# Kernel optimization log

Measured on AMD Instinct MI355X. Metric: run time of the kernel, lower is better.

The kernel has to match this reference:

```python
import jax, jax.numpy as jnp
import numpy as np

D_MODEL = 1024
N_HEADS = 16
HEAD_DIM = D_MODEL // N_HEADS
B, L, E = 2, 2048, 256


def _linear_params(key, d_out, d_in):
    kw, kb = jax.random.split(key)
    lim = 1.0 / np.sqrt(d_in)
    W = jax.random.uniform(kw, (d_out, d_in), jnp.float32, -lim, lim)
    b = jax.random.uniform(kb, (d_out,), jnp.float32, -lim, lim)
    return W, b


def setup_inputs() -> dict:
    key = jax.random.key(0)
    ks = jax.random.split(key, 10)
    x = jax.random.normal(ks[0], (B, L, D_MODEL), jnp.float32)
    kg_embeds = jax.random.normal(ks[1], (B, E, D_MODEL), jnp.float32)
    Wq, bq = _linear_params(ks[2], D_MODEL, D_MODEL)
    Wk, bk = _linear_params(ks[3], D_MODEL, D_MODEL)
    Wv, bv = _linear_params(ks[4], D_MODEL, D_MODEL)
    Wo, bo = _linear_params(ks[5], D_MODEL, D_MODEL)
    Wkk, bkk = _linear_params(ks[6], D_MODEL, D_MODEL)
    Wkv, bkv = _linear_params(ks[7], D_MODEL, D_MODEL)
    Wg, bg = _linear_params(ks[8], D_MODEL, 2 * D_MODEL)
    return {"x": x, "kg_embeds": kg_embeds,
            "Wq": Wq, "bq": bq, "Wk": Wk, "bk": bk, "Wv": Wv, "bv": bv,
            "Wkk": Wkk, "bkk": bkk, "Wkv": Wkv, "bkv": bkv,
            "Wo": Wo, "bo": bo, "Wg": Wg, "bg": bg}


def _heads(t):
    # [B, S, D] -> [B, H, S, hd]
    Bb, S, _ = t.shape
    return t.reshape(Bb, S, N_HEADS, HEAD_DIM).transpose(0, 2, 1, 3)


def reference(x, kg_embeds, Wq, bq, Wk, bk, Wv, bv, Wkk, bkk, Wkv, bkv, Wo, bo, Wg, bg):
    scale = HEAD_DIM ** -0.5
    q = _heads(x @ Wq.T + bq)                      # [B,H,L,hd]
    k = _heads(x @ Wk.T + bk)
    v = _heads(x @ Wv.T + bv)
    k_kg = _heads(kg_embeds @ Wkk.T + bkk)         # [B,H,E,hd]
    v_kg = _heads(kg_embeds @ Wkv.T + bkv)
    k_aug = jnp.concatenate([k, k_kg], axis=2)     # [B,H,L+E,hd]
    v_aug = jnp.concatenate([v, v_kg], axis=2)
    scores = jnp.einsum('bhld,bhmd->bhlm', q, k_aug) * scale  # [B,H,L,L+E]
    attn = jax.nn.softmax(scores, axis=-1)
    out = jnp.einsum('bhlm,bhmd->bhld', attn, v_aug)           # [B,H,L,hd]
    out = out.transpose(0, 2, 1, 3).reshape(x.shape)            # [B,L,D]
    kg_global = jnp.broadcast_to(kg_embeds.mean(axis=1, keepdims=True), x.shape)
    gate = jax.nn.sigmoid(jnp.concatenate([out, kg_global], axis=-1) @ Wg.T + bg)
    return gate * (out @ Wo.T + bo) + (1.0 - gate) * x
```

## Files before the change

### kernel.cpp

```cpp
#include <hip/hip_runtime.h>
#include <stdint.h>

typedef unsigned short ushort_t;
typedef __attribute__((ext_vector_type(8))) short short8;
typedef __attribute__((ext_vector_type(4))) short short4v;
typedef __attribute__((ext_vector_type(4))) float f32x4;
typedef __attribute__((ext_vector_type(4))) unsigned uintx4;

#define DEV static __device__ __forceinline__

DEV unsigned short f2bf(float f) {
  unsigned u = __builtin_bit_cast(unsigned, f);
  u += 0x7fffu + ((u >> 16) & 1u);
  return (unsigned short)(u >> 16);
}
DEV float bf2f(unsigned short b) {
  return __builtin_bit_cast(float, (unsigned)b << 16);
}

DEV void gl16(const void* g, void* l) {
  __builtin_amdgcn_global_load_lds(
      (__attribute__((address_space(1))) char*)(unsigned long long)g,
      (__attribute__((address_space(3))) char*)(unsigned)(unsigned long long)l,
      16, 0, 0);
}

DEV f32x4 mfma_bf16(short8 a, short8 b, f32x4 c) {
  return __builtin_amdgcn_mfma_f32_16x16x32_bf16(a, b, c, 0, 0, 0);
}

DEV unsigned cvtpk(float lo, float hi) {
  unsigned r;
  asm("v_cvt_pk_bf16_f32 %0, %1, %2" : "=v"(r) : "v"(lo), "v"(hi));
  return r;
}
DEV void swap_net(unsigned& a, unsigned& b) {
  asm("v_permlane32_swap_b32 %0, %1" : "+v"(a), "+v"(b));
  asm("v_permlane16_swap_b32 %0, %1" : "+v"(a), "+v"(b));
}
DEV float redmax4(float x) {
  unsigned a = __builtin_bit_cast(unsigned, x), b = a;
  asm("v_permlane16_swap_b32 %0, %1" : "+v"(a), "+v"(b));
  float y = fmaxf(__builtin_bit_cast(float, a), __builtin_bit_cast(float, b));
  unsigned c = __builtin_bit_cast(unsigned, y), d = c;
  asm("v_permlane32_swap_b32 %0, %1" : "+v"(c), "+v"(d));
  return fmaxf(__builtin_bit_cast(float, c), __builtin_bit_cast(float, d));
}
DEV float lanebcast(float v, int srclane) {
  return __builtin_bit_cast(float,
      __builtin_amdgcn_ds_bpermute(srclane * 4, __builtin_bit_cast(int, v)));
}

__global__ __launch_bounds__(256) void k_cvt_all(
    const float* __restrict__ x, const float* __restrict__ kg,
    const float* __restrict__ Wq, const float* __restrict__ Wk, const float* __restrict__ Wv,
    const float* __restrict__ Wkk, const float* __restrict__ Wkv,
    const float* __restrict__ Wo, const float* __restrict__ Wg,
    ushort_t* __restrict__ xh, ushort_t* __restrict__ kgh,
    ushort_t* __restrict__ WB1, ushort_t* __restrict__ WB2, ushort_t* __restrict__ WB3) {
  const int b = blockIdx.x;
  if (b >= 10752) {
    const int i = (b - 10752) * 256 + threadIdx.x;
    const int r = i >> 8, c = (i & 255) * 4;
    const float4 v = *(const float4*)(Wg + (size_t)r * 2048 + c);
    short4v o;
    o.x = (short)f2bf(v.x); o.y = (short)f2bf(v.y); o.z = (short)f2bf(v.z); o.w = (short)f2bf(v.w);
    *(short4v*)(WB3 + 1048576 + (size_t)r * 1024 + c) = o;
    return;
  }
  const float* src;
  ushort_t* dst;
  int off;
  if (b < 4096)       { src = x;   dst = xh;            off = b; }
  else if (b < 4608)  { src = kg;  dst = kgh;           off = b - 4096; }
  else if (b < 5632)  { src = Wq;  dst = WB1;           off = b - 4608; }
  else if (b < 6656)  { src = Wk;  dst = WB1 + 1048576; off = b - 5632; }
  else if (b < 7680)  { src = Wv;  dst = WB1 + 2097152; off = b - 6656; }
  else if (b < 8704)  { src = Wkk; dst = WB2;           off = b - 7680; }
  else if (b < 9728)  { src = Wkv; dst = WB2 + 1048576; off = b - 8704; }
  else                { src = Wo;  dst = WB3;           off = b - 9728; }
  const int i = off * 1024 + threadIdx.x * 4;
  const float4 v = *(const float4*)(src + i);
  short4v o;
  o.x = (short)f2bf(v.x); o.y = (short)f2bf(v.y); o.z = (short)f2bf(v.z); o.w = (short)f2bf(v.w);
  *(short4v*)(dst + i) = o;
}

__global__ __launch_bounds__(256) void k_kgmean(const float* __restrict__ kg, float* __restrict__ out) {
  const int i = blockIdx.x * 256 + threadIdx.x;
  const int b = i >> 10, d = i & 1023;
  float s = 0.f;
  #pragma unroll 4
  for (int e = 0; e < 256; e++) s += kg[((size_t)b * 256 + e) * 1024 + d];
  out[i] = s * (1.0f / 256.0f);
}

__global__ __launch_bounds__(256) void k_g2(const float* __restrict__ kgm, const float* __restrict__ Wg,
                                            const float* __restrict__ bg, float* __restrict__ g2) {
  const int w = threadIdx.x >> 6, l = threadIdx.x & 63;
  const int idx = blockIdx.x * 4 + w;
  const int b = idx >> 10, n = idx & 1023;
  const float* wr = Wg + (size_t)n * 2048 + 1024;
  const float* mb = kgm + b * 1024;
  float s = 0.f;
  #pragma unroll
  for (int j = 0; j < 16; j++) s += mb[j * 64 + l] * wr[j * 64 + l];
  #pragma unroll
  for (int m = 32; m >= 1; m >>= 1) s += __shfl_xor(s, m);
  if (l == 0) g2[idx] = s + bg[n];
}

__global__ __launch_bounds__(256, 3) void k_mm128(
    const ushort_t* __restrict__ A0, const ushort_t* __restrict__ B0,
    const ushort_t* __restrict__ A1, const ushort_t* __restrict__ B1,
    const float* __restrict__ f0, const float* __restrict__ f1, const float* __restrict__ f2,
    const float* __restrict__ f3, const float* __restrict__ f4,
    ushort_t* __restrict__ o0, ushort_t* __restrict__ o1, ushort_t* __restrict__ o2) {
  __shared__ __align__(16) char SHb[49152];
  const int tid = threadIdx.x;
  const int w = tid >> 6, l = tid & 63;
  const int wr = w >> 1, wc = w & 1;
  const int fr = l & 15, fg = l >> 4;

  int m0, n0, iskg = 0;
  {
    const int wg = ((int)blockIdx.x & 7) * 104 + ((int)blockIdx.x >> 3);
    if (wg < 768) { m0 = (wg / 24) * 128; n0 = (wg % 24) * 128; }
    else          { const int k = wg - 768; iskg = 1; m0 = (k >> 4) * 128; n0 = (k & 15) * 128; }
  }
  const ushort_t* A = iskg ? A1 : A0;
  const ushort_t* B = iskg ? B1 : B0;

  int grow[2], gcb[2];
  #pragma unroll
  for (int j = 0; j < 2; j++) {
    const int beta = j * 256 + tid;
    const int rp = beta >> 3;
    const int u = (beta & 7) ^ (rp & 7);
    grow[j] = 2 * rp + (u >> 2);
    gcb[j] = u & 3;
  }
  const char* gA[2];
  const char* gB[2];
  #pragma unroll
  for (int j = 0; j < 2; j++) {
    gA[j] = (const char*)A + (size_t)(m0 + grow[j]) * 2048 + gcb[j] * 16;
    gB[j] = (const char*)B + (size_t)(n0 + grow[j]) * 2048 + gcb[j] * 16;
  }

  auto stage = [&](int s, int kt) {
    char* As = SHb + s * 16384;
    char* Bs = As + 8192;
    const int ko = kt * 64;
    #pragma unroll
    for (int j = 0; j < 2; j++) {
      gl16(gA[j] + ko, As + j * 4096 + tid * 16);
      gl16(gB[j] + ko, Bs + j * 4096 + tid * 16);
    }
  };

  int aoff[4], boff[4];
  #pragma unroll
  for (int i = 0; i < 4; i++) {
    const int rowa = wr * 64 + i * 16 + fr;
    aoff[i] = (rowa >> 1) * 128 + ((((rowa & 1) << 6) | (fg << 4)) ^ (((rowa >> 1) & 7) << 4));
    const int rowb = wc * 64 + i * 16 + fr;
    boff[i] = (rowb >> 1) * 128 + ((((rowb & 1) << 6) | (fg << 4)) ^ (((rowb >> 1) & 7) << 4));
  }

  f32x4 acc[4][4] = {};

  stage(0, 0);
  stage(1, 1);
  int sc = 0, sn2 = 2;
  for (int kt = 0; kt < 32; kt++) {
    if (kt < 31) asm volatile("s_waitcnt vmcnt(4)" ::: "memory");
    else         asm volatile("s_waitcnt vmcnt(0)" ::: "memory");
    __builtin_amdgcn_s_barrier();
    asm volatile("" ::: "memory");
    if (kt < 30) stage(sn2, kt + 2);
    const char* Ab = SHb + sc * 16384;
    const char* Bb = Ab + 8192;
    short8 af[4], bf[4];
    #pragma unroll
    for (int j = 0; j < 4; j++) bf[j] = *(const short8*)(Bb + boff[j]);
    #pragma unroll
    for (int i = 0; i < 4; i++) af[i] = *(const short8*)(Ab + aoff[i]);
    __builtin_amdgcn_s_setprio(1);
    #pragma unroll
    for (int i = 0; i < 4; i++)
      #pragma unroll
      for (int j = 0; j < 4; j++)
        acc[i][j] = mfma_bf16(af[i], bf[j], acc[i][j]);
    __builtin_amdgcn_s_setprio(0);
    sc++; if (sc == 3) sc = 0;
    sn2++; if (sn2 == 3) sn2 = 0;
  }
  __syncthreads();

  const int sec = n0 >> 10;
  const bool isV = (!iskg && sec == 2) || (iskg && sec == 1);

  if (isV) {
    ushort_t* SHs = (ushort_t*)SHb;
    const float* bV = iskg ? f4 : f2;
    const int bidx = iskg ? (m0 >> 8) : (m0 >> 11);
    const int colbase = iskg ? (2048 + (m0 & 255)) : (m0 & 2047);
    #pragma unroll
    for (int i = 0; i < 4; i++) {
      #pragma unroll
      for (int j = 0; j < 4; j++) {
        const int nl = wc * 64 + j * 16 + fr;
        const int ml0 = wr * 64 + i * 16 + fg * 4;
        const float bb = bV[(n0 & 1023) + nl];
        short4v pk;
        #pragma unroll
        for (int r = 0; r < 4; r++) pk[r] = (short)f2bf(acc[i][j][r] + bb);
        *(short4v*)(SHs + nl * 128 + (ml0 ^ ((nl & 7) << 3))) = pk;
      }
    }
    __syncthreads();
    const int row = tid >> 1, half = tid & 1;
    const int h = ((n0 & 1023) >> 6) + (row >> 6);
    const int d = row & 63;
    ushort_t* dst = o2 + ((size_t)(bidx * 16 + h) * 64 + d) * 2304 + colbase + half * 64;
    const ushort_t* srow2 = SHs + row * 128;
    #pragma unroll
    for (int k2 = 0; k2 < 8; k2++) {
      const int me = (half * 64 + k2 * 8) ^ ((row & 7) << 3);
      *(short8*)(dst + k2 * 8) = *(const short8*)(srow2 + me);
    }
    return;
  }

  #pragma unroll
  for (int i = 0; i < 4; i++) {
    #pragma unroll
    for (int j = 0; j < 4; j++) {
      const int nn = (n0 & 1023) + wc * 64 + j * 16 + fr;
      const int h = nn >> 6, d = nn & 63;
      #pragma unroll
      for (int r = 0; r < 4; r++) {
        const int m = m0 + wr * 64 + i * 16 + fg * 4 + r;
        const float v = acc[i][j][r];
        if (iskg) {
          const int b = m >> 8, e = m & 255;
          o1[((size_t)(b * 16 + h) * 2304 + 2048 + e) * 64 + d] = f2bf(v + f3[nn]);
        } else if (sec == 0) {
          const int b = m >> 11, lq = m & 2047;
          o0[((size_t)(b * 16 + h) * 2048 + lq) * 64 + d] = f2bf((v + f0[nn]) * 0.18033688f);
        } else {
          const int b = m >> 11, lq = m & 2047;
          o1[((size_t)(b * 16 + h) * 2304 + lq) * 64 + d] = f2bf(v + f1[nn]);
        }
      }
    }
  }
}

__global__ __launch_bounds__(256, 2) void k_mmout(
    const ushort_t* __restrict__ Og, const ushort_t* __restrict__ WB3,
    const float* __restrict__ bo, const float* __restrict__ g2v,
    const float* __restrict__ x, float* __restrict__ y) {
  __shared__ __align__(16) char SHb[61440];
  const int tid = threadIdx.x;
  const int w = tid >> 6, l = tid & 63;
  const int wr = w >> 1, wc = w & 1;
  const int fr = l & 15, fg = l >> 4;

  const int wg = ((int)blockIdx.x & 7) * 64 + ((int)blockIdx.x >> 3);
  const int m0 = (wg >> 3) * 64, n0 = (wg & 7) * 128;

  const int rpA = tid >> 3, uA = (tid & 7) ^ (rpA & 7);
  const char* gAp = (const char*)Og + (size_t)(m0 + 2 * rpA + (uA >> 2)) * 2048 + (uA & 3) * 16;
  int grow[2], gcb[2];
  #pragma unroll
  for (int j = 0; j < 2; j++) {
    const int beta = j * 256 + tid;
    const int rp = beta >> 3;
    const int u = (beta & 7) ^ (rp & 7);
    grow[j] = 2 * rp + (u >> 2);
    gcb[j] = u & 3;
  }
  const char* gBo[2];
  const char* gBg[2];
  #pragma unroll
  for (int j = 0; j < 2; j++) {
    gBo[j] = (const char*)WB3 + (size_t)(n0 + grow[j]) * 2048 + gcb[j] * 16;
    gBg[j] = (const char*)(WB3 + 1048576) + (size_t)(n0 + grow[j]) * 2048 + gcb[j] * 16;
  }

  auto stage = [&](int s, int kt) {
    char* As = SHb + s * 20480;
    const int ko = kt * 64;
    gl16(gAp + ko, As + tid * 16);
    #pragma unroll
    for (int j = 0; j < 2; j++) {
      gl16(gBo[j] + ko, As + 4096 + j * 4096 + tid * 16);
      gl16(gBg[j] + ko, As + 12288 + j * 4096 + tid * 16);
    }
  };

  int aoff[2], boff[4];
  #pragma unroll
  for (int i = 0; i < 2; i++) {
    const int rowa = wr * 32 + i * 16 + fr;
    aoff[i] = (rowa >> 1) * 128 + ((((rowa & 1) << 6) | (fg << 4)) ^ (((rowa >> 1) & 7) << 4));
  }
  #pragma unroll
  for (int j = 0; j < 4; j++) {
    const int rowb = wc * 64 + j * 16 + fr;
    boff[j] = (rowb >> 1) * 128 + ((((rowb & 1) << 6) | (fg << 4)) ^ (((rowb >> 1) & 7) << 4));
  }

  f32x4 ao[2][4] = {};
  f32x4 ag[2][4] = {};

  stage(0, 0);
  stage(1, 1);
  int sc = 0, sn2 = 2;
  for (int kt = 0; kt < 32; kt++) {
    if (kt < 31) asm volatile("s_waitcnt vmcnt(5)" ::: "memory");
    else         asm volatile("s_waitcnt vmcnt(0)" ::: "memory");
    __builtin_amdgcn_s_barrier();
    asm volatile("" ::: "memory");
    if (kt < 30) stage(sn2, kt + 2);
    const char* Ab = SHb + sc * 20480;
    short8 af[2], bof[4], bgf[4];
    #pragma unroll
    for (int i = 0; i < 2; i++) af[i] = *(const short8*)(Ab + aoff[i]);
    #pragma unroll
    for (int j = 0; j < 4; j++) {
      bof[j] = *(const short8*)(Ab + 4096 + boff[j]);
      bgf[j] = *(const short8*)(Ab + 12288 + boff[j]);
    }
    __builtin_amdgcn_s_setprio(1);
    #pragma unroll
    for (int i = 0; i < 2; i++)
      #pragma unroll
      for (int j = 0; j < 4; j++) {
        ao[i][j] = mfma_bf16(af[i], bof[j], ao[i][j]);
        ag[i][j] = mfma_bf16(af[i], bgf[j], ag[i][j]);
      }
    __builtin_amdgcn_s_setprio(0);
    sc++; if (sc == 3) sc = 0;
    sn2++; if (sn2 == 3) sn2 = 0;
  }

  const int bidx = m0 >> 11;
  #pragma unroll
  for (int i = 0; i < 2; i++) {
    #pragma unroll
    for (int j = 0; j < 4; j++) {
      const int nn = n0 + wc * 64 + j * 16 + fr;
      const float bb = bo[nn];
      const float gg = g2v[bidx * 1024 + nn];
      #pragma unroll
      for (int r = 0; r < 4; r++) {
        const int m = m0 + wr * 32 + i * 16 + fg * 4 + r;
        const float co = ao[i][j][r] + bb;
        const float cg = ag[i][j][r] + gg;
        const float gate = 1.0f / (1.0f + __builtin_amdgcn_exp2f(cg * -1.4426950408889634f));
        const float xv = x[(size_t)m * 1024 + nn];
        y[(size_t)m * 1024 + nn] = xv + gate * (co - xv);
      }
    }
  }
}

__global__ __launch_bounds__(256, 4) void k_attn(
    const ushort_t* __restrict__ Qg, const ushort_t* __restrict__ Kg,
    const ushort_t* __restrict__ Vtg, ushort_t* __restrict__ Og) {
  __shared__ __align__(16) ushort_t Ks[2][64 * 64];
  __shared__ __align__(16) ushort_t Vs[2][64 * 64];
  const int tid = threadIdx.x;
  const int w = tid >> 6, l = tid & 63;
  const int fr = l & 15, fg = l >> 4;

  const int id = blockIdx.y * gridDim.x + blockIdx.x;
  const int bh = (id & 7) * 4 + ((id >> 3) >> 5);
  const int q0 = ((id >> 3) & 31) * 64 + w * 16;

  short8 qf[2];
  {
    const short* qrow = (const short*)(Qg + ((size_t)bh * 2048 + q0 + fr) * 64);
    qf[0] = *(const short8*)(qrow + fg * 8);
    qf[1] = *(const short8*)(qrow + 32 + fg * 8);
  }

  constexpr short ONE = 0x3F80;
  const short8 ones = {ONE, ONE, ONE, ONE, ONE, ONE, ONE, ONE};

  f32x4 o[4] = {};
  f32x4 lacc = {};
  float mrun = -1.0e30f;

  const int rsub = tid >> 3;
  const int cS = ((tid & 7) * 16) ^ ((rsub & 7) << 4);
  const char* kbase = (const char*)(Kg + (size_t)bh * 2304 * 64);
  const char* vbase = (const char*)(Vtg + (size_t)bh * 64 * 2304);

  auto stage = [&](int nb, int tile) {
    #pragma unroll
    for (int j = 0; j < 2; j++) {
      const int row = j * 32 + rsub;
      gl16(kbase + (size_t)(tile * 64 + row) * 128 + cS,
           (char*)&Ks[nb][0] + j * 4096 + tid * 16);
      gl16(vbase + (size_t)row * 4608 + tile * 128 + cS,
           (char*)&Vs[nb][0] + j * 4096 + tid * 16);
    }
  };

  stage(0, 0);

  const int rswz = (fr & 7) << 4;

  for (int mt = 0; mt < 36; mt++) {
    __syncthreads();
    if (mt < 35) stage((mt + 1) & 1, mt + 1);

    const char* Kb = (const char*)&Ks[mt & 1][0];
    const char* Vb = (const char*)&Vs[mt & 1][0];

    f32x4 s[4];
    #pragma unroll
    for (int t = 0; t < 4; t++) {
      const int rb = (t * 16 + fr) * 128 + fg * 16;
      const short8 k0 = *(const short8*)(Kb + (rb ^ rswz));
      const short8 k1 = *(const short8*)(Kb + ((rb + 64) ^ rswz));
      f32x4 z = {};
      z = mfma_bf16(k0, qf[0], z);
      z = mfma_bf16(k1, qf[1], z);
      s[t] = z;
    }

    float m = fmaxf(s[0][0], s[0][1]);
    m = fmaxf(fmaxf(m, s[0][2]), s[0][3]);
    m = fmaxf(fmaxf(m, s[1][0]), s[1][1]);
    m = fmaxf(fmaxf(m, s[1][2]), s[1][3]);
    m = fmaxf(fmaxf(m, s[2][0]), s[2][1]);
    m = fmaxf(fmaxf(m, s[2][2]), s[2][3]);
    m = fmaxf(fmaxf(m, s[3][0]), s[3][1]);
    m = fmaxf(fmaxf(m, s[3][2]), s[3][3]);
    const float mx = redmax4(m);
    if (__any(mx - mrun > 11.5416f)) {
      const float mn = fmaxf(mrun, mx);
      const float al = __builtin_amdgcn_exp2f(mrun - mn);
      mrun = mn;
      float ab[4];
      #pragma unroll
      for (int r = 0; r < 4; r++) ab[r] = lanebcast(al, fg * 4 + r);
      #pragma unroll
      for (int r = 0; r < 4; r++) {
        lacc[r] *= ab[r];
        #pragma unroll
        for (int dt = 0; dt < 4; dt++) o[dt][r] *= ab[r];
      }
    }
    #pragma unroll
    for (int t = 0; t < 4; t++)
      #pragma unroll
      for (int r = 0; r < 4; r++)
        s[t][r] = __builtin_amdgcn_exp2f(s[t][r] - mrun);

    #pragma unroll
    for (int c = 0; c < 2; c++) {
      unsigned a0 = cvtpk(s[2 * c][0], s[2 * c][1]);
      unsigned b0 = cvtpk(s[2 * c + 1][0], s[2 * c + 1][1]);
      unsigned a1 = cvtpk(s[2 * c][2], s[2 * c][3]);
      unsigned b1 = cvtpk(s[2 * c + 1][2], s[2 * c + 1][3]);
      swap_net(a0, b0);
      swap_net(a1, b1);
      uintx4 u;
      u.x = a0; u.y = a1; u.z = b0; u.w = b1;
      const short8 pf = __builtin_bit_cast(short8, u);
      lacc = mfma_bf16(pf, ones, lacc);
      #pragma unroll
      for (int dt = 0; dt < 4; dt++) {
        const int vb2 = ((dt * 16 + fr) * 128) + fg * 16 + c * 64;
        const short8 vf = *(const short8*)(Vb + (vb2 ^ rswz));
        o[dt] = mfma_bf16(pf, vf, o[dt]);
      }
    }
  }

  const int b = bh >> 4, h = bh & 15;
  #pragma unroll
  for (int r = 0; r < 4; r++) {
    const float inv = 1.0f / lacc[r];
    const int q = q0 + fg * 4 + r;
    ushort_t* orow = Og + ((size_t)b * 2048 + q) * 1024 + h * 64;
    #pragma unroll
    for (int dt = 0; dt < 4; dt++) orow[dt * 16 + fr] = f2bf(o[dt][r] * inv);
  }
}

extern "C" void kernel_launch(void* const* d_in, const int* in_sizes, int n_in,
                              void* d_out, int out_size, void* d_ws, size_t ws_size,
                              hipStream_t stream) {
  (void)in_sizes; (void)n_in; (void)out_size; (void)ws_size;
  const float* x   = (const float*)d_in[0];
  const float* kg  = (const float*)d_in[1];
  const float* Wq  = (const float*)d_in[2];
  const float* bq  = (const float*)d_in[3];
  const float* Wk  = (const float*)d_in[4];
  const float* bk  = (const float*)d_in[5];
  const float* Wv  = (const float*)d_in[6];
  const float* bv  = (const float*)d_in[7];
  const float* Wkk = (const float*)d_in[8];
  const float* bkk = (const float*)d_in[9];
  const float* Wkv = (const float*)d_in[10];
  const float* bkv = (const float*)d_in[11];
  const float* Wo  = (const float*)d_in[12];
  const float* bo  = (const float*)d_in[13];
  const float* Wg  = (const float*)d_in[14];
  const float* bg  = (const float*)d_in[15];
  float* y = (float*)d_out;

  char* ws = (char*)d_ws;
  size_t off = 0;
  auto take = [&](size_t bytes) {
    char* p = ws + off;
    off += (bytes + 255) & ~(size_t)255;
    return p;
  };
  ushort_t* xh   = (ushort_t*)take((size_t)4096 * 1024 * 2);
  ushort_t* kgh  = (ushort_t*)take((size_t)512 * 1024 * 2);
  ushort_t* WB1  = (ushort_t*)take((size_t)3072 * 1024 * 2);
  ushort_t* WB2  = (ushort_t*)take((size_t)2048 * 1024 * 2);
  ushort_t* WB3  = (ushort_t*)take((size_t)2048 * 1024 * 2);
  ushort_t* Qg   = (ushort_t*)take((size_t)32 * 2048 * 64 * 2);
  ushort_t* Kaug = (ushort_t*)take((size_t)32 * 2304 * 64 * 2);
  ushort_t* Vt   = (ushort_t*)take((size_t)32 * 2304 * 64 * 2);
  ushort_t* Og   = (ushort_t*)take((size_t)4096 * 1024 * 2);
  float* kgm     = (float*)take(2048 * 4);
  float* g2      = (float*)take(2048 * 4);

  k_cvt_all<<<11776, 256, 0, stream>>>(x, kg, Wq, Wk, Wv, Wkk, Wkv, Wo, Wg,
                                       xh, kgh, WB1, WB2, WB3);
  k_kgmean<<<8, 256, 0, stream>>>(kg, kgm);
  k_g2<<<512, 256, 0, stream>>>(kgm, Wg, bg, g2);

  k_mm128<<<832, 256, 0, stream>>>(xh, WB1, kgh, WB2,
                                   bq, bk, bv, bkk, bkv, Qg, Kaug, Vt);
  k_attn<<<dim3(32, 32), 256, 0, stream>>>(Qg, Kaug, Vt, Og);
  k_mmout<<<512, 256, 0, stream>>>(Og, WB3, bo, g2, x, y);
}
```

Before: 177.1 us.

## Replace QKV projection GEMM with 256x256-tile, 8-wave, double-buffered pipelined kernel

Rewrites the fused Q/K/V/KG projection GEMM to use 256x256 output tiles with 512 threads (8 waves, each computing 128x64), a K-step of 64 with double-buffered 64KB LDS stages, and LDS reads interleaved with MFMA quads and global-to-LDS loads under fine-grained barriers. Larger tiles raise arithmetic intensity and cut global/L2 traffic, and the interleaved schedule is meant to overlap loads with compute. The cost is a grid of only 208 blocks on a 256-CU device, so some CUs sit idle. It also uses 128KB of LDS per block and many barriers per iteration, which limits occupancy.

```diff
diff --git a/kernel.cpp b/kernel.cpp
--- a/kernel.cpp
+++ b/kernel.cpp
@@ -110,148 +110,191 @@
   if (l == 0) g2[idx] = s + bg[n];
 }
 
-__global__ __launch_bounds__(256, 3) void k_mm128(
-    const ushort_t* __restrict__ A0, const ushort_t* __restrict__ B0,
-    const ushort_t* __restrict__ A1, const ushort_t* __restrict__ B1,
-    const float* __restrict__ f0, const float* __restrict__ f1, const float* __restrict__ f2,
-    const float* __restrict__ f3, const float* __restrict__ f4,
-    ushort_t* __restrict__ o0, ushort_t* __restrict__ o1, ushort_t* __restrict__ o2) {
-  __shared__ __align__(16) char SHb[49152];
+#define BARm() do { __builtin_amdgcn_s_barrier(); asm volatile("" ::: "memory"); } while (0)
+
+#define RD_A(DST, SBASE, IOFF)                                      \
+  _Pragma("unroll")                                                 \
+  for (int i = 0; i < 4; i++) {                                     \
+    DST[i][0] = *(const short8*)((SBASE) + aoff[(IOFF) + i]);       \
+    DST[i][1] = *(const short8*)((SBASE) + (aoff[(IOFF) + i] ^ 64));\
+  }
+#define RD_B(DST, SBASE, JOFF)                                      \
+  _Pragma("unroll")                                                 \
+  for (int j = 0; j < 2; j++) {                                     \
+    DST[j][0] = *(const short8*)((SBASE) + boff[(JOFF) + j]);       \
+    DST[j][1] = *(const short8*)((SBASE) + (boff[(JOFF) + j] ^ 64));\
+  }
+#define MFMA_QUAD(AF, BF, I0, J0)                                   \
+  __builtin_amdgcn_s_setprio(1);                                    \
+  _Pragma("unroll")                                                 \
+  for (int i = 0; i < 4; i++) {                                     \
+    _Pragma("unroll")                                               \
+    for (int j = 0; j < 2; j++) {                                   \
+      acc[(I0) + i][(J0) + j] = mfma_bf16(AF[i][0], BF[j][0], acc[(I0) + i][(J0) + j]); \
+      acc[(I0) + i][(J0) + j] = mfma_bf16(AF[i][1], BF[j][1], acc[(I0) + i][(J0) + j]); \
+    }                                                               \
+  }                                                                 \
+  __builtin_amdgcn_s_setprio(0);
+
+__global__ __launch_bounds__(512, 2) void k_mmqkv(
+    const ushort_t* __restrict__ xh, const ushort_t* __restrict__ WB1,
+    const ushort_t* __restrict__ kgh, const ushort_t* __restrict__ WB2,
+    const float* __restrict__ bq, const float* __restrict__ bk, const float* __restrict__ bv,
+    const float* __restrict__ bkk, const float* __restrict__ bkv,
+    ushort_t* __restrict__ Qg, ushort_t* __restrict__ Kaug, ushort_t* __restrict__ Vt) {
+  __shared__ __align__(16) char SHb[131072];
   const int tid = threadIdx.x;
   const int w = tid >> 6, l = tid & 63;
-  const int wr = w >> 1, wc = w & 1;
+  const int wr = w >> 2, wc = w & 3;
   const int fr = l & 15, fg = l >> 4;
 
-  int m0, n0, iskg = 0;
-  {
-    const int wg = ((int)blockIdx.x & 7) * 104 + ((int)blockIdx.x >> 3);
-    if (wg < 768) { m0 = (wg / 24) * 128; n0 = (wg % 24) * 128; }
-    else          { const int k = wg - 768; iskg = 1; m0 = (k >> 4) * 128; n0 = (k & 15) * 128; }
-  }
-  const ushort_t* A = iskg ? A1 : A0;
-  const ushort_t* B = iskg ? B1 : B0;
-
-  int grow[2], gcb[2];
-  #pragma unroll
-  for (int j = 0; j < 2; j++) {
-    const int beta = j * 256 + tid;
-    const int rp = beta >> 3;
-    const int u = (beta & 7) ^ (rp & 7);
-    grow[j] = 2 * rp + (u >> 2);
-    gcb[j] = u & 3;
-  }
-  const char* gA[2];
-  const char* gB[2];
-  #pragma unroll
-  for (int j = 0; j < 2; j++) {
-    gA[j] = (const char*)A + (size_t)(m0 + grow[j]) * 2048 + gcb[j] * 16;
-    gB[j] = (const char*)B + (size_t)(n0 + grow[j]) * 2048 + gcb[j] * 16;
-  }
-
-  auto stage = [&](int s, int kt) {
-    char* As = SHb + s * 16384;
-    char* Bs = As + 8192;
-    const int ko = kt * 64;
-    #pragma unroll
-    for (int j = 0; j < 2; j++) {
-      gl16(gA[j] + ko, As + j * 4096 + tid * 16);
-      gl16(gB[j] + ko, Bs + j * 4096 + tid * 16);
-    }
+  int m0, by, iskg = 0;
+  const int wg = ((int)blockIdx.x & 7) * 26 + ((int)blockIdx.x >> 3);
+  if (wg < 192) { m0 = (wg / 12) * 256; by = wg % 12; }
+  else          { const int k = wg - 192; iskg = 1; by = k & 7; m0 = (k >> 3) * 256; }
+  const int n0 = by * 256;
+  const ushort_t* A = iskg ? kgh : xh;
+  const ushort_t* B = iskg ? WB2 : WB1;
+
+  const int rIH = tid >> 3;
+  const int cc = (tid & 7) ^ (rIH & 7);
+  const char* gA = (const char*)A + (size_t)(m0 + rIH) * 2048 + cc * 16;
+  const char* gB = (const char*)B + (size_t)(n0 + rIH) * 2048 + cc * 16;
+
+  auto stg = [&](int slot, int ab, int h, int kt) {
+    const char* g = (ab ? gB : gA) + (size_t)h * 262144 + kt * 128;
+    char* d = SHb + (slot << 16) + ab * 32768 + h * 16384 + tid * 16;
+    gl16(g, d);
+    gl16(g + 131072, d + 8192);
   };
 
-  int aoff[4], boff[4];
-  #pragma unroll
-  for (int i = 0; i < 4; i++) {
-    const int rowa = wr * 64 + i * 16 + fr;
-    aoff[i] = (rowa >> 1) * 128 + ((((rowa & 1) << 6) | (fg << 4)) ^ (((rowa >> 1) & 7) << 4));
-    const int rowb = wc * 64 + i * 16 + fr;
-    boff[i] = (rowb >> 1) * 128 + ((((rowb & 1) << 6) | (fg << 4)) ^ (((rowb >> 1) & 7) << 4));
-  }
-
-  f32x4 acc[4][4] = {};
-
-  stage(0, 0);
-  stage(1, 1);
-  int sc = 0, sn2 = 2;
-  for (int kt = 0; kt < 32; kt++) {
-    if (kt < 31) asm volatile("s_waitcnt vmcnt(4)" ::: "memory");
-    else         asm volatile("s_waitcnt vmcnt(0)" ::: "memory");
-    __builtin_amdgcn_s_barrier();
-    asm volatile("" ::: "memory");
-    if (kt < 30) stage(sn2, kt + 2);
-    const char* Ab = SHb + sc * 16384;
-    const char* Bb = Ab + 8192;
-    short8 af[4], bf[4];
-    #pragma unroll
-    for (int j = 0; j < 4; j++) bf[j] = *(const short8*)(Bb + boff[j]);
-    #pragma unroll
-    for (int i = 0; i < 4; i++) af[i] = *(const short8*)(Ab + aoff[i]);
-    __builtin_amdgcn_s_setprio(1);
-    #pragma unroll
-    for (int i = 0; i < 4; i++)
-      #pragma unroll
-      for (int j = 0; j < 4; j++)
-        acc[i][j] = mfma_bf16(af[i], bf[j], acc[i][j]);
-    __builtin_amdgcn_s_setprio(0);
-    sc++; if (sc == 3) sc = 0;
-    sn2++; if (sn2 == 3) sn2 = 0;
+  const int swz = (fg ^ (fr & 7)) * 16;
+  int aoff[8], boff[4];
+  #pragma unroll
+  for (int i = 0; i < 8; i++)
+    aoff[i] = wr * 16384 + (i * 16 + fr) * 128 + swz;
+  #pragma unroll
+  for (int j = 0; j < 4; j++)
+    boff[j] = 32768 + (wc >> 1) * 16384 + ((wc & 1) * 64 + j * 16 + fr) * 128 + swz;
+
+  f32x4 acc[8][4] = {};
+
+  stg(0, 0, 0, 0); stg(0, 0, 1, 0); stg(0, 1, 0, 0); stg(0, 1, 1, 0);
+  stg(1, 0, 0, 1); stg(1, 0, 1, 1);
+  asm volatile("s_waitcnt vmcnt(4)" ::: "memory");
+  BARm();
+
+  const char* S0 = SHb;
+  const char* S1 = SHb + 65536;
+
+  for (int it = 0; it < 8; ++it) {
+    const int t = 2 * it;
+    const bool pre = (t < 14);
+    short8 a0[4][2], a1[4][2], b0[2][2], b1[2][2];
+
+    RD_A(a0, S0, 0)
+    RD_B(b0, S0, 0)
+    stg(1, 1, 0, t + 1);
+    BARm();
+    MFMA_QUAD(a0, b0, 0, 0)
+    BARm();
+    RD_A(a1, S0, 4)
+    stg(1, 1, 1, t + 1);
+    BARm();
+    MFMA_QUAD(a1, b0, 4, 0)
+    BARm();
+    RD_B(b1, S0, 2)
+    if (pre) stg(0, 0, 0, t + 2);
+    BARm();
+    MFMA_QUAD(a1, b1, 4, 2)
+    BARm();
+    if (pre) stg(0, 0, 1, t + 2);
+    BARm();
+    MFMA_QUAD(a0, b1, 0, 2)
+    if (pre) asm volatile("s_waitcnt vmcnt(4)" ::: "memory");
+    else     asm volatile("s_waitcnt vmcnt(0)" ::: "memory");
+    BARm();
+
+    RD_A(a0, S1, 0)
+    RD_B(b0, S1, 0)
+    if (pre) stg(0, 1, 0, t + 2);
+    BARm();
+    MFMA_QUAD(a0, b0, 0, 0)
+    BARm();
+    RD_A(a1, S1, 4)
+    if (pre) stg(0, 1, 1, t + 2);
+    BARm();
+    MFMA_QUAD(a1, b0, 4, 0)
+    BARm();
+    RD_B(b1, S1, 2)
+    if (pre) stg(1, 0, 0, t + 3);
+    BARm();
+    MFMA_QUAD(a1, b1, 4, 2)
+    BARm();
+    if (pre) stg(1, 0, 1, t + 3);
+    BARm();
+    MFMA_QUAD(a0, b1, 0, 2)
+    if (pre) asm volatile("s_waitcnt vmcnt(4)" ::: "memory");
+    else     asm volatile("s_waitcnt vmcnt(0)" ::: "memory");
+    BARm();
   }
   __syncthreads();
 
-  const int sec = n0 >> 10;
-  const bool isV = (!iskg && sec == 2) || (iskg && sec == 1);
+  const int sec = iskg ? (by >> 2) + 10 : (by >> 2);
+  const int nnbase = (by & 3) * 256;
+  const bool isV = (sec == 2 || sec == 11);
 
   if (isV) {
     ushort_t* SHs = (ushort_t*)SHb;
-    const float* bV = iskg ? f4 : f2;
+    const float* bV = iskg ? bkv : bv;
     const int bidx = iskg ? (m0 >> 8) : (m0 >> 11);
     const int colbase = iskg ? (2048 + (m0 & 255)) : (m0 & 2047);
     #pragma unroll
-    for (int i = 0; i < 4; i++) {
+    for (int i = 0; i < 8; i++) {
       #pragma unroll
       for (int j = 0; j < 4; j++) {
         const int nl = wc * 64 + j * 16 + fr;
-        const int ml0 = wr * 64 + i * 16 + fg * 4;
-        const float bb = bV[(n0 & 1023) + nl];
+        const int ml0 = wr * 128 + i * 16 + fg * 4;
+        const float bb = bV[nnbase + nl];
         short4v pk;
         #pragma unroll
         for (int r = 0; r < 4; r++) pk[r] = (short)f2bf(acc[i][j][r] + bb);
-        *(short4v*)(SHs + nl * 128 + (ml0 ^ ((nl & 7) << 3))) = pk;
+        *(short4v*)(SHs + nl * 256 + (ml0 ^ ((nl & 7) << 3))) = pk;
       }
     }
     __syncthreads();
-    const int row = tid >> 1, half = tid & 1;
-    const int h = ((n0 & 1023) >> 6) + (row >> 6);
-    const int d = row & 63;
-    ushort_t* dst = o2 + ((size_t)(bidx * 16 + h) * 64 + d) * 2304 + colbase + half * 64;
-    const ushort_t* srow2 = SHs + row * 128;
-    #pragma unroll
-    for (int k2 = 0; k2 < 8; k2++) {
-      const int me = (half * 64 + k2 * 8) ^ ((row & 7) << 3);
-      *(short8*)(dst + k2 * 8) = *(const short8*)(srow2 + me);
+    const int nl = tid >> 1, mh = tid & 1;
+    const int n = nnbase + nl;
+    const int h = n >> 6, d = n & 63;
+    ushort_t* dst = Vt + ((size_t)(bidx * 16 + h) * 64 + d) * 2304 + colbase + mh * 128;
+    const ushort_t* srcr = SHs + nl * 256;
+    #pragma unroll
+    for (int k2 = 0; k2 < 16; k2++) {
+      const int me = (mh * 128 + k2 * 8) ^ ((nl & 7) << 3);
+      *(short8*)(dst + k2 * 8) = *(const short8*)(srcr + me);
     }
     return;
   }
 
   #pragma unroll
-  for (int i = 0; i < 4; i++) {
+  for (int i = 0; i < 8; i++) {
     #pragma unroll
     for (int j = 0; j < 4; j++) {
-      const int nn = (n0 & 1023) + wc * 64 + j * 16 + fr;
+      const int nn = nnbase + wc * 64 + j * 16 + fr;
       const int h = nn >> 6, d = nn & 63;
       #pragma unroll
       for (int r = 0; r < 4; r++) {
-        const int m = m0 + wr * 64 + i * 16 + fg * 4 + r;
+        const int m = m0 + wr * 128 + i * 16 + fg * 4 + r;
         const float v = acc[i][j][r];
-        if (iskg) {
+        if (sec == 0) {
+          const int b = m >> 11, lq = m & 2047;
+          Qg[((size_t)(b * 16 + h) * 2048 + lq) * 64 + d] = f2bf((v + bq[nn]) * 0.18033688f);
+        } else if (sec == 1) {
+          const int b = m >> 11, lq = m & 2047;
+          Kaug[((size_t)(b * 16 + h) * 2304 + lq) * 64 + d] = f2bf(v + bk[nn]);
+        } else {
           const int b = m >> 8, e = m & 255;
-          o1[((size_t)(b * 16 + h) * 2304 + 2048 + e) * 64 + d] = f2bf(v + f3[nn]);
-        } else if (sec == 0) {
-          const int b = m >> 11, lq = m & 2047;
-          o0[((size_t)(b * 16 + h) * 2048 + lq) * 64 + d] = f2bf((v + f0[nn]) * 0.18033688f);
-        } else {
-          const int b = m >> 11, lq = m & 2047;
-          o1[((size_t)(b * 16 + h) * 2304 + lq) * 64 + d] = f2bf(v + f1[nn]);
+          Kaug[((size_t)(b * 16 + h) * 2304 + 2048 + e) * 64 + d] = f2bf(v + bkk[nn]);
         }
       }
     }
@@ -541,7 +584,7 @@
   k_kgmean<<<8, 256, 0, stream>>>(kg, kgm);
   k_g2<<<512, 256, 0, stream>>>(kgm, Wg, bg, g2);
 
-  k_mm128<<<832, 256, 0, stream>>>(xh, WB1, kgh, WB2,
+  k_mmqkv<<<208, 512, 0, stream>>>(xh, WB1, kgh, WB2,
                                    bq, bk, bv, bkk, bkv, Qg, Kaug, Vt);
   k_attn<<<dim3(32, 32), 256, 0, stream>>>(Qg, Kaug, Vt, Og);
   k_mmout<<<512, 256, 0, stream>>>(Og, WB3, bo, g2, x, y);
```

Measured after the change: 193.3 us. 1.09x slower.
